# Kernel tuning notes

Hardware: AMD Instinct MI355X
Metric: run time of the kernel (lower is better)

## Reference

```python
import jax, jax.numpy as jnp
import numpy as np

EPS = 1e-12  # torch F.normalize eps
ALPHA = 100.0


def _l2norm(v, axis):
    n = jnp.sqrt(jnp.sum(v * v, axis=axis, keepdims=True))
    return v / jnp.maximum(n, EPS)


def setup_inputs() -> dict:
    key = jax.random.key(0)
    kx, kc = jax.random.split(key)
    B, D, H, W, K = 16, 512, 64, 64, 64
    x = jax.random.normal(kx, (B, D, H, W), dtype=jnp.float32)
    centroids = jax.random.uniform(kc, (K, D), dtype=jnp.float32)
    # NetVLAD._init_params: conv weight/bias derived from centroids at init
    conv_w = 2.0 * ALPHA * centroids                 # [K, D] (1x1 conv kernel)
    conv_b = -ALPHA * jnp.linalg.norm(centroids, axis=1)  # [K]
    return {"x": x, "centroids": centroids, "conv_w": conv_w, "conv_b": conv_b}


def reference(x, centroids, conv_w, conv_b):
    B, D = x.shape[:2]
    K = centroids.shape[0]
    # descriptor-wise L2 normalization over channel dim
    x = _l2norm(x, axis=1)
    xf = x.reshape(B, D, -1)                          # [B, D, N]
    # 1x1 conv == per-position matmul: [B, K, N]
    logits = jnp.einsum('kd,bdn->bkn', conv_w, xf) + conv_b[None, :, None]
    assign = jax.nn.softmax(logits, axis=1)           # soft assignment over K
    # vlad[b,k,d] = sum_n a[b,k,n]*(x[b,d,n] - c[k,d])
    #            = (a @ x^T) - a.sum(n) * c   (avoids B*K*D*N intermediate)
    agg = jnp.einsum('bkn,bdn->bkd', assign, xf)      # [B, K, D]
    mass = jnp.sum(assign, axis=-1)                   # [B, K]
    vlad = agg - mass[..., None] * centroids[None]    # [B, K, D]
    vlad = _l2norm(vlad, axis=2)                      # intra-normalization
    vlad = vlad.reshape(B, -1)                        # [B, K*D]
    return _l2norm(vlad, axis=1)
```

## Files before the change

kernel.cpp:

```cpp
#include <hip/hip_runtime.h>
#include <cstddef>

constexpr int Bn = 16, Dn = 512, Nn = 4096, Kn = 64;
constexpr int PN = 128;
constexpr int NP = Nn / PN;
constexpr int Dp = 520;
constexpr float FEPS = 1e-12f;

typedef __bf16 bf16x8 __attribute__((ext_vector_type(8)));
typedef float f32x4 __attribute__((ext_vector_type(4)));

__device__ __forceinline__ unsigned short bf_bits(__bf16 h) {
  union { __bf16 b; unsigned short u; } c;
  c.b = h;
  return c.u;
}

__global__ __launch_bounds__(256) void kW(const float* __restrict__ w,
                                          unsigned short* __restrict__ w_hi,
                                          unsigned short* __restrict__ w_lo) {
  const int idx = blockIdx.x * 256 + threadIdx.x;
  const float v = w[idx];
  const __bf16 h = (__bf16)v;
  const float r = v - (float)h;
  const __bf16 l = (__bf16)r;
  w_hi[idx] = bf_bits(h);
  w_lo[idx] = bf_bits(l);
}

__global__ __launch_bounds__(512, 4) void kF(const float* __restrict__ x,
                                             const unsigned short* __restrict__ w_hi,
                                             const unsigned short* __restrict__ w_lo,
                                             const float* __restrict__ conv_b,
                                             float* __restrict__ aggp,
                                             float* __restrict__ massp) {
  __shared__ float smem[2 * PN * 33];
  __shared__ float msum[8][64];
  const int tid = threadIdx.x;
  const int l = tid & 63;
  const int wv = tid >> 6;
  const int ll = l & 15;
  const int lg = l >> 4;
  const int b = blockIdx.x >> 5;
  const int p = blockIdx.x & 31;
  const int n0 = p << 7;
  const float* xb = x + (size_t)b * Dn * Nn + n0;

  f32x4 acc[4];
#pragma unroll
  for (int kt = 0; kt < 4; ++kt) acc[kt] = (f32x4){0.f, 0.f, 0.f, 0.f};
  float ss = 0.f;

  const int srow = tid >> 4;
  const int sc0 = (tid & 15) << 3;
  float4 pf0 = *(const float4*)(xb + (size_t)srow * Nn + sc0);
  float4 pf1 = *(const float4*)(xb + (size_t)srow * Nn + sc0 + 4);

  for (int dc = 0; dc < Dn; dc += 32) {
    float* xs = smem + ((dc >> 5) & 1) * (PN * 33);
    xs[(sc0 + 0) * 33 + srow] = pf0.x;
    xs[(sc0 + 1) * 33 + srow] = pf0.y;
    xs[(sc0 + 2) * 33 + srow] = pf0.z;
    xs[(sc0 + 3) * 33 + srow] = pf0.w;
    xs[(sc0 + 4) * 33 + srow] = pf1.x;
    xs[(sc0 + 5) * 33 + srow] = pf1.y;
    xs[(sc0 + 6) * 33 + srow] = pf1.z;
    xs[(sc0 + 7) * 33 + srow] = pf1.w;
    if (dc + 32 < Dn) {
      pf0 = *(const float4*)(xb + (size_t)(dc + 32 + srow) * Nn + sc0);
      pf1 = *(const float4*)(xb + (size_t)(dc + 32 + srow) * Nn + sc0 + 4);
    }
    __syncthreads();

    const int ncol = (wv << 4) + ll;
    const float* xcol = xs + ncol * 33 + lg * 8;
    float xv[8];
#pragma unroll
    for (int j = 0; j < 8; ++j) xv[j] = xcol[j];
    bf16x8 bh, bl;
#pragma unroll
    for (int j = 0; j < 8; ++j) {
      ss = fmaf(xv[j], xv[j], ss);
      const __bf16 h = (__bf16)xv[j];
      bh[j] = h;
      bl[j] = (__bf16)(xv[j] - (float)h);
    }
#pragma unroll
    for (int kt = 0; kt < 4; ++kt) {
      const size_t woff = (size_t)(kt * 16 + ll) * Dn + dc + lg * 8;
      bf16x8 ah = *(const bf16x8*)(w_hi + woff);
      bf16x8 al = *(const bf16x8*)(w_lo + woff);
      acc[kt] = __builtin_amdgcn_mfma_f32_16x16x32_bf16(ah, bh, acc[kt], 0, 0, 0);
      acc[kt] = __builtin_amdgcn_mfma_f32_16x16x32_bf16(ah, bl, acc[kt], 0, 0, 0);
      acc[kt] = __builtin_amdgcn_mfma_f32_16x16x32_bf16(al, bh, acc[kt], 0, 0, 0);
    }
  }

  ss += __shfl_xor(ss, 16);
  ss += __shfl_xor(ss, 32);
  const float iv = 1.f / fmaxf(sqrtf(ss), FEPS);
  float lgt[16];
#pragma unroll
  for (int kt = 0; kt < 4; ++kt)
#pragma unroll
    for (int r = 0; r < 4; ++r)
      lgt[kt * 4 + r] = fmaf(acc[kt][r], iv, conv_b[kt * 16 + lg * 4 + r]);
  float pmax = lgt[0];
#pragma unroll
  for (int i = 1; i < 16; ++i) pmax = fmaxf(pmax, lgt[i]);
  pmax = fmaxf(pmax, __shfl_xor(pmax, 16));
  pmax = fmaxf(pmax, __shfl_xor(pmax, 32));
  float ex[16];
  float psum = 0.f;
#pragma unroll
  for (int i = 0; i < 16; ++i) {
    ex[i] = expf(lgt[i] - pmax);
    psum += ex[i];
  }
  psum += __shfl_xor(psum, 16);
  psum += __shfl_xor(psum, 32);
  const float isum = 1.f / psum;

  __syncthreads();

  unsigned short* as_hi = (unsigned short*)smem;
  unsigned short* as_lo = as_hi + PN * Kn;
  const int ngb = (wv << 1) + (ll >> 3);
  const int jj = ll & 7;
#pragma unroll
  for (int i = 0; i < 16; ++i) {
    const int k = (i >> 2) * 16 + lg * 4 + (i & 3);
    const float a = ex[i] * isum;
    const float v = a * iv;
    const __bf16 h = (__bf16)v;
    as_hi[(ngb * 64 + k) * 8 + jj] = bf_bits(h);
    as_lo[(ngb * 64 + k) * 8 + jj] = bf_bits((__bf16)(v - (float)h));
    float m = a;
    m += __shfl_xor(m, 1);
    m += __shfl_xor(m, 2);
    m += __shfl_xor(m, 4);
    m += __shfl_xor(m, 8);
    if (ll == 0) msum[wv][k] = m;
  }
  __syncthreads();
  if (tid < 64) {
    float s = 0.f;
#pragma unroll
    for (int ww = 0; ww < 8; ++ww) s += msum[ww][tid];
    massp[((b << 5) + p) * Kn + tid] = s;
  }

  f32x4 acc2[4][4];
#pragma unroll
  for (int kt = 0; kt < 4; ++kt)
#pragma unroll
    for (int dt = 0; dt < 4; ++dt) acc2[kt][dt] = (f32x4){0.f, 0.f, 0.f, 0.f};

  const float* xq = x + (size_t)b * Dn * Nn +
                    (size_t)(wv * 64 + ll) * Nn + n0 + lg * 8;

#pragma unroll
  for (int nc = 0; nc < PN; nc += 32) {
    const int ng = (nc >> 3) + lg;
    bf16x8 af_h[4], af_l[4];
#pragma unroll
    for (int kt = 0; kt < 4; ++kt) {
      const int idx = (ng * 64 + kt * 16 + ll) * 8;
      af_h[kt] = *(const bf16x8*)(as_hi + idx);
      af_l[kt] = *(const bf16x8*)(as_lo + idx);
    }
    bf16x8 bx[4];
#pragma unroll
    for (int dt = 0; dt < 4; ++dt) {
      const float* xr = xq + (size_t)(dt * 16) * Nn + nc;
      float4 x0 = *(const float4*)(xr);
      float4 x1 = *(const float4*)(xr + 4);
      bx[dt][0] = (__bf16)x0.x; bx[dt][1] = (__bf16)x0.y;
      bx[dt][2] = (__bf16)x0.z; bx[dt][3] = (__bf16)x0.w;
      bx[dt][4] = (__bf16)x1.x; bx[dt][5] = (__bf16)x1.y;
      bx[dt][6] = (__bf16)x1.z; bx[dt][7] = (__bf16)x1.w;
    }
#pragma unroll
    for (int kt = 0; kt < 4; ++kt)
#pragma unroll
      for (int dt = 0; dt < 4; ++dt) {
        acc2[kt][dt] = __builtin_amdgcn_mfma_f32_16x16x32_bf16(
            af_h[kt], bx[dt], acc2[kt][dt], 0, 0, 0);
        acc2[kt][dt] = __builtin_amdgcn_mfma_f32_16x16x32_bf16(
            af_l[kt], bx[dt], acc2[kt][dt], 0, 0, 0);
      }
  }

  float* outb = aggp + (size_t)((b << 5) + p) * Kn * Dp;
#pragma unroll
  for (int kt = 0; kt < 4; ++kt)
#pragma unroll
    for (int dt = 0; dt < 4; ++dt) {
      const int krow = kt * 16 + (lg << 2);
      const int dcol = wv * 64 + dt * 16 + ll;
      float* op = outb + (size_t)krow * Dp + dcol;
#pragma unroll
      for (int r = 0; r < 4; ++r) op[(size_t)r * Dp] = acc2[kt][dt][r];
    }
}

__device__ __forceinline__ float blockReduceSum(float v, float* sb) {
#pragma unroll
  for (int off = 32; off > 0; off >>= 1) v += __shfl_down(v, off, 64);
  const int lane = threadIdx.x & 63, w = threadIdx.x >> 6;
  if (lane == 0) sb[w] = v;
  __syncthreads();
  if (threadIdx.x == 0) sb[4] = sb[0] + sb[1] + sb[2] + sb[3];
  __syncthreads();
  return sb[4];
}

__global__ __launch_bounds__(256) void kC1(const float* __restrict__ massp,
                                           const float* __restrict__ aggp,
                                           const float* __restrict__ centroids,
                                           float* __restrict__ out,
                                           float* __restrict__ rowsq) {
  __shared__ float sb[5];
  const int tid = threadIdx.x;
  const int b = blockIdx.x >> 6, k = blockIdx.x & 63;
  float s = 0.f;
  if (tid < 32) s = massp[((b << 5) + tid) * Kn + k];
  const float mass = blockReduceSum(s, sb);
  float v[2];
  float sq = 0.f;
#pragma unroll
  for (int u = 0; u < 2; ++u) {
    const int d = tid + (u << 8);
    float val = -mass * centroids[k * Dn + d];
#pragma unroll 8
    for (int pp = 0; pp < 32; ++pp)
      val += aggp[((size_t)((b << 5) + pp) * Kn + k) * Dp + d];
    v[u] = val;
    sq = fmaf(val, val, sq);
  }
  const float rsq = blockReduceSum(sq, sb);
  const float inv = 1.f / fmaxf(sqrtf(rsq), FEPS);
#pragma unroll
  for (int u = 0; u < 2; ++u)
    out[((size_t)b * Kn + k) * Dn + tid + (u << 8)] = v[u] * inv;
  if (tid == 0) rowsq[b * Kn + k] = rsq * inv * inv;
}

__global__ __launch_bounds__(256) void kC2(float* __restrict__ out,
                                           const float* __restrict__ rowsq) {
  __shared__ float sg;
  const int b = blockIdx.x, tid = threadIdx.x;
  float v = (tid < 64) ? rowsq[b * Kn + tid] : 0.f;
  if (tid < 64) {
#pragma unroll
    for (int off = 32; off > 0; off >>= 1) v += __shfl_down(v, off, 64);
  }
  if (tid == 0) sg = 1.f / fmaxf(sqrtf(v), FEPS);
  __syncthreads();
  const float inv = sg;
  float* ob = out + (size_t)b * (Kn * Dn);
  for (int t = tid; t < Kn * Dn; t += 256) ob[t] *= inv;
}

extern "C" void kernel_launch(void* const* d_in, const int* in_sizes, int n_in,
                              void* d_out, int out_size, void* d_ws,
                              size_t ws_size, hipStream_t stream) {
  const float* x = (const float*)d_in[0];
  const float* centroids = (const float*)d_in[1];
  const float* conv_w = (const float*)d_in[2];
  const float* conv_b = (const float*)d_in[3];
  float* out = (float*)d_out;
  float* ws = (float*)d_ws;
  float* aggp = ws;
  unsigned short* w_hi = (unsigned short*)(ws + 17039360);
  unsigned short* w_lo = (unsigned short*)(ws + 17055744);
  float* massp = ws + 17072128;
  float* rowsq = ws + 17104896;

  kW<<<128, 256, 0, stream>>>(conv_w, w_hi, w_lo);
  kF<<<512, 512, 0, stream>>>(x, w_hi, w_lo, conv_b, aggp, massp);
  kC1<<<1024, 256, 0, stream>>>(massp, aggp, centroids, out, rowsq);
  kC2<<<16, 256, 0, stream>>>(out, rowsq);
}
```

Baseline: 143.4 us.

## Stage 64-channel x tiles with two-deep register prefetch and fewer barriers

The x staging in the fused kernel now transposes 64 channels per step instead of 32, with two register prefetch sets that alternate between two shared buffers. This halves the number of barriers and gives each thread larger 16-float global loads. It also swaps __syncthreads for a raw lgkmcnt wait plus s_barrier. The costs are double the LDS footprint (about 67KB plus msum), which may cut occupancy under launch_bounds(512,4), and higher register pressure from 32 prefetch floats.

```diff
diff --git a/kernel.cpp b/kernel.cpp
--- a/kernel.cpp
+++ b/kernel.cpp
@@ -3,7 +3,6 @@
 
 constexpr int Bn = 16, Dn = 512, Nn = 4096, Kn = 64;
 constexpr int PN = 128;
-constexpr int NP = Nn / PN;
 constexpr int Dp = 520;
 constexpr float FEPS = 1e-12f;
 
@@ -34,7 +33,7 @@
                                              const float* __restrict__ conv_b,
                                              float* __restrict__ aggp,
                                              float* __restrict__ massp) {
-  __shared__ float smem[2 * PN * 33];
+  __shared__ float smem[2 * PN * 66];
   __shared__ float msum[8][64];
   const int tid = threadIdx.x;
   const int l = tid & 63;
@@ -51,50 +50,79 @@
   for (int kt = 0; kt < 4; ++kt) acc[kt] = (f32x4){0.f, 0.f, 0.f, 0.f};
   float ss = 0.f;
 
-  const int srow = tid >> 4;
-  const int sc0 = (tid & 15) << 3;
-  float4 pf0 = *(const float4*)(xb + (size_t)srow * Nn + sc0);
-  float4 pf1 = *(const float4*)(xb + (size_t)srow * Nn + sc0 + 4);
-
-  for (int dc = 0; dc < Dn; dc += 32) {
-    float* xs = smem + ((dc >> 5) & 1) * (PN * 33);
-    xs[(sc0 + 0) * 33 + srow] = pf0.x;
-    xs[(sc0 + 1) * 33 + srow] = pf0.y;
-    xs[(sc0 + 2) * 33 + srow] = pf0.z;
-    xs[(sc0 + 3) * 33 + srow] = pf0.w;
-    xs[(sc0 + 4) * 33 + srow] = pf1.x;
-    xs[(sc0 + 5) * 33 + srow] = pf1.y;
-    xs[(sc0 + 6) * 33 + srow] = pf1.z;
-    xs[(sc0 + 7) * 33 + srow] = pf1.w;
-    if (dc + 32 < Dn) {
-      pf0 = *(const float4*)(xb + (size_t)(dc + 32 + srow) * Nn + sc0);
-      pf1 = *(const float4*)(xb + (size_t)(dc + 32 + srow) * Nn + sc0 + 4);
-    }
-    __syncthreads();
-
-    const int ncol = (wv << 4) + ll;
-    const float* xcol = xs + ncol * 33 + lg * 8;
-    float xv[8];
-#pragma unroll
-    for (int j = 0; j < 8; ++j) xv[j] = xcol[j];
-    bf16x8 bh, bl;
-#pragma unroll
-    for (int j = 0; j < 8; ++j) {
-      ss = fmaf(xv[j], xv[j], ss);
-      const __bf16 h = (__bf16)xv[j];
-      bh[j] = h;
-      bl[j] = (__bf16)(xv[j] - (float)h);
-    }
-#pragma unroll
-    for (int kt = 0; kt < 4; ++kt) {
-      const size_t woff = (size_t)(kt * 16 + ll) * Dn + dc + lg * 8;
-      bf16x8 ah = *(const bf16x8*)(w_hi + woff);
-      bf16x8 al = *(const bf16x8*)(w_lo + woff);
-      acc[kt] = __builtin_amdgcn_mfma_f32_16x16x32_bf16(ah, bh, acc[kt], 0, 0, 0);
-      acc[kt] = __builtin_amdgcn_mfma_f32_16x16x32_bf16(ah, bl, acc[kt], 0, 0, 0);
-      acc[kt] = __builtin_amdgcn_mfma_f32_16x16x32_bf16(al, bh, acc[kt], 0, 0, 0);
-    }
-  }
+  const int srow = tid >> 3;
+  const int sc0 = (tid & 7) << 4;
+  const float* xsrc = xb + (size_t)srow * Nn + sc0;
+  const int ncol = (wv << 4) + ll;
+
+  float4 pfA[4], pfB[4];
+#pragma unroll
+  for (int q = 0; q < 4; ++q) pfA[q] = *(const float4*)(xsrc + 4 * q);
+#pragma unroll
+  for (int q = 0; q < 4; ++q)
+    pfB[q] = *(const float4*)(xsrc + (size_t)64 * Nn + 4 * q);
+
+#define KF_CONSUME(XS, DC)                                                    \
+  {                                                                           \
+    const float* xcol = (XS) + ncol * 66;                                     \
+    _Pragma("unroll") for (int s = 0; s < 2; ++s) {                           \
+      float xv[8];                                                            \
+      _Pragma("unroll") for (int j = 0; j < 8; ++j)                           \
+          xv[j] = xcol[s * 32 + lg * 8 + j];                                  \
+      bf16x8 bh, bl;                                                          \
+      _Pragma("unroll") for (int j = 0; j < 8; ++j) {                         \
+        ss = fmaf(xv[j], xv[j], ss);                                          \
+        const __bf16 h = (__bf16)xv[j];                                       \
+        bh[j] = h;                                                            \
+        bl[j] = (__bf16)(xv[j] - (float)h);                                   \
+      }                                                                       \
+      _Pragma("unroll") for (int kt = 0; kt < 4; ++kt) {                      \
+        const size_t woff = (size_t)(kt * 16 + ll) * Dn + (DC) + s * 32 + lg * 8; \
+        bf16x8 ah = *(const bf16x8*)(w_hi + woff);                            \
+        bf16x8 al = *(const bf16x8*)(w_lo + woff);                            \
+        acc[kt] = __builtin_amdgcn_mfma_f32_16x16x32_bf16(ah, bh, acc[kt], 0, 0, 0); \
+        acc[kt] = __builtin_amdgcn_mfma_f32_16x16x32_bf16(ah, bl, acc[kt], 0, 0, 0); \
+        acc[kt] = __builtin_amdgcn_mfma_f32_16x16x32_bf16(al, bh, acc[kt], 0, 0, 0); \
+      }                                                                       \
+    }                                                                         \
+  }
+
+#pragma unroll
+  for (int it = 0; it < 4; ++it) {
+    {
+      float* xs = smem;
+#pragma unroll
+      for (int q = 0; q < 4; ++q)
+#pragma unroll
+        for (int j = 0; j < 4; ++j)
+          xs[(sc0 + 4 * q + j) * 66 + srow] = ((const float*)&pfA[q])[j];
+      if (it < 3) {
+#pragma unroll
+        for (int q = 0; q < 4; ++q)
+          pfA[q] = *(const float4*)(xsrc + (size_t)(it * 128 + 128) * Nn + 4 * q);
+      }
+      asm volatile("s_waitcnt lgkmcnt(0)" ::: "memory");
+      __builtin_amdgcn_s_barrier();
+      KF_CONSUME(xs, it * 128);
+    }
+    {
+      float* xs = smem + PN * 66;
+#pragma unroll
+      for (int q = 0; q < 4; ++q)
+#pragma unroll
+        for (int j = 0; j < 4; ++j)
+          xs[(sc0 + 4 * q + j) * 66 + srow] = ((const float*)&pfB[q])[j];
+      if (it < 3) {
+#pragma unroll
+        for (int q = 0; q < 4; ++q)
+          pfB[q] = *(const float4*)(xsrc + (size_t)(it * 128 + 192) * Nn + 4 * q);
+      }
+      asm volatile("s_waitcnt lgkmcnt(0)" ::: "memory");
+      __builtin_amdgcn_s_barrier();
+      KF_CONSUME(xs, it * 128 + 64);
+    }
+  }
+#undef KF_CONSUME
 
   ss += __shfl_xor(ss, 16);
   ss += __shfl_xor(ss, 32);
```

Measured after the change: 150.1 us. 1.05x slower.

## Cache bf16 x tile in LDS, drop second x read, process two chunks per block

Applied to the files above, without the earlier changes.

The fused kernel now keeps a swizzled bf16 copy of the whole 512x128 x tile in LDS during the first pass. The aggregation GEMM reads x from LDS instead of reloading it from global memory. The low half of the assignment split is dropped, so the second GEMM uses single-bf16 assignments. Each block handles two N-chunks and accumulates them into one partial, which halves the partial aggregate buffer and the reduction work in kC1. The cost is a large LDS footprint (about 128KB), which lowers occupancy, plus a small loss of precision in the assignment weights.

```diff
diff --git a/kernel.cpp b/kernel.cpp
--- a/kernel.cpp
+++ b/kernel.cpp
@@ -3,7 +3,6 @@
 
 constexpr int Bn = 16, Dn = 512, Nn = 4096, Kn = 64;
 constexpr int PN = 128;
-constexpr int NP = Nn / PN;
 constexpr int Dp = 520;
 constexpr float FEPS = 1e-12f;
 
@@ -28,170 +27,164 @@
   w_lo[idx] = bf_bits(l);
 }
 
-__global__ __launch_bounds__(512, 4) void kF(const float* __restrict__ x,
+__global__ __launch_bounds__(512, 2) void kF(const float* __restrict__ x,
                                              const unsigned short* __restrict__ w_hi,
                                              const unsigned short* __restrict__ w_lo,
                                              const float* __restrict__ conv_b,
                                              float* __restrict__ aggp,
                                              float* __restrict__ massp) {
-  __shared__ float smem[2 * PN * 33];
+  __shared__ float xs[PN * 33];
+  __shared__ unsigned short xhi[Dn * PN];
   __shared__ float msum[8][64];
   const int tid = threadIdx.x;
   const int l = tid & 63;
   const int wv = tid >> 6;
   const int ll = l & 15;
   const int lg = l >> 4;
-  const int b = blockIdx.x >> 5;
-  const int p = blockIdx.x & 31;
-  const int n0 = p << 7;
-  const float* xb = x + (size_t)b * Dn * Nn + n0;
-
-  f32x4 acc[4];
-#pragma unroll
-  for (int kt = 0; kt < 4; ++kt) acc[kt] = (f32x4){0.f, 0.f, 0.f, 0.f};
-  float ss = 0.f;
-
+  const int b = blockIdx.x >> 4;
+  const int sp = blockIdx.x & 15;
   const int srow = tid >> 4;
   const int sc0 = (tid & 15) << 3;
-  float4 pf0 = *(const float4*)(xb + (size_t)srow * Nn + sc0);
-  float4 pf1 = *(const float4*)(xb + (size_t)srow * Nn + sc0 + 4);
-
-  for (int dc = 0; dc < Dn; dc += 32) {
-    float* xs = smem + ((dc >> 5) & 1) * (PN * 33);
-    xs[(sc0 + 0) * 33 + srow] = pf0.x;
-    xs[(sc0 + 1) * 33 + srow] = pf0.y;
-    xs[(sc0 + 2) * 33 + srow] = pf0.z;
-    xs[(sc0 + 3) * 33 + srow] = pf0.w;
-    xs[(sc0 + 4) * 33 + srow] = pf1.x;
-    xs[(sc0 + 5) * 33 + srow] = pf1.y;
-    xs[(sc0 + 6) * 33 + srow] = pf1.z;
-    xs[(sc0 + 7) * 33 + srow] = pf1.w;
-    if (dc + 32 < Dn) {
-      pf0 = *(const float4*)(xb + (size_t)(dc + 32 + srow) * Nn + sc0);
-      pf1 = *(const float4*)(xb + (size_t)(dc + 32 + srow) * Nn + sc0 + 4);
-    }
+  const int ncol = (wv << 4) + ll;
+
+  f32x4 acc2[4][4];
+#pragma unroll
+  for (int kt = 0; kt < 4; ++kt)
+#pragma unroll
+    for (int dt = 0; dt < 4; ++dt) acc2[kt][dt] = (f32x4){0.f, 0.f, 0.f, 0.f};
+
+  for (int rep = 0; rep < 2; ++rep) {
+    const int p = (sp << 1) + rep;
+    const int n0 = p << 7;
+    const float* xbp = x + (size_t)b * Dn * Nn + n0;
+
+    f32x4 acc[4];
+#pragma unroll
+    for (int kt = 0; kt < 4; ++kt) acc[kt] = (f32x4){0.f, 0.f, 0.f, 0.f};
+    float ss = 0.f;
+
+    float4 pf0 = *(const float4*)(xbp + (size_t)srow * Nn + sc0);
+    float4 pf1 = *(const float4*)(xbp + (size_t)srow * Nn + sc0 + 4);
+
+    for (int dc = 0; dc < Dn; dc += 32) {
+      const float pv[8] = {pf0.x, pf0.y, pf0.z, pf0.w, pf1.x, pf1.y, pf1.z, pf1.w};
+#pragma unroll
+      for (int j = 0; j < 8; ++j) xs[(sc0 + j) * 33 + srow] = pv[j];
+      {
+        unsigned short hb[8];
+#pragma unroll
+        for (int j = 0; j < 8; ++j) hb[j] = bf_bits((__bf16)pv[j]);
+        const unsigned byteoff =
+            (unsigned)(((dc + srow) * PN + sc0) * 2) ^ ((unsigned)(srow & 7) << 4);
+        uint4 hv;
+        hv.x = (unsigned)hb[0] | ((unsigned)hb[1] << 16);
+        hv.y = (unsigned)hb[2] | ((unsigned)hb[3] << 16);
+        hv.z = (unsigned)hb[4] | ((unsigned)hb[5] << 16);
+        hv.w = (unsigned)hb[6] | ((unsigned)hb[7] << 16);
+        *(uint4*)((char*)xhi + byteoff) = hv;
+      }
+      if (dc + 32 < Dn) {
+        pf0 = *(const float4*)(xbp + (size_t)(dc + 32 + srow) * Nn + sc0);
+        pf1 = *(const float4*)(xbp + (size_t)(dc + 32 + srow) * Nn + sc0 + 4);
+      }
+      asm volatile("s_waitcnt lgkmcnt(0)\ns_barrier" ::: "memory");
+
+      float xv[8];
+#pragma unroll
+      for (int j = 0; j < 8; ++j) xv[j] = xs[ncol * 33 + lg * 8 + j];
+      bf16x8 bh, bl;
+#pragma unroll
+      for (int j = 0; j < 8; ++j) {
+        ss = fmaf(xv[j], xv[j], ss);
+        const __bf16 h = (__bf16)xv[j];
+        bh[j] = h;
+        bl[j] = (__bf16)(xv[j] - (float)h);
+      }
+#pragma unroll
+      for (int kt = 0; kt < 4; ++kt) {
+        const size_t woff = (size_t)(kt * 16 + ll) * Dn + dc + lg * 8;
+        bf16x8 ah = *(const bf16x8*)(w_hi + woff);
+        bf16x8 al = *(const bf16x8*)(w_lo + woff);
+        acc[kt] = __builtin_amdgcn_mfma_f32_16x16x32_bf16(ah, bh, acc[kt], 0, 0, 0);
+        acc[kt] = __builtin_amdgcn_mfma_f32_16x16x32_bf16(ah, bl, acc[kt], 0, 0, 0);
+        acc[kt] = __builtin_amdgcn_mfma_f32_16x16x32_bf16(al, bh, acc[kt], 0, 0, 0);
+      }
+      asm volatile("s_waitcnt lgkmcnt(0)\ns_barrier" ::: "memory");
+    }
+
+    ss += __shfl_xor(ss, 16);
+    ss += __shfl_xor(ss, 32);
+    const float iv = 1.f / fmaxf(sqrtf(ss), FEPS);
+    float lgt[16];
+#pragma unroll
+    for (int kt = 0; kt < 4; ++kt)
+#pragma unroll
+      for (int r = 0; r < 4; ++r)
+        lgt[kt * 4 + r] = fmaf(acc[kt][r], iv, conv_b[kt * 16 + lg * 4 + r]);
+    float pmax = lgt[0];
+#pragma unroll
+    for (int i = 1; i < 16; ++i) pmax = fmaxf(pmax, lgt[i]);
+    pmax = fmaxf(pmax, __shfl_xor(pmax, 16));
+    pmax = fmaxf(pmax, __shfl_xor(pmax, 32));
+    float ex[16];
+    float psum = 0.f;
+#pragma unroll
+    for (int i = 0; i < 16; ++i) {
+      ex[i] = expf(lgt[i] - pmax);
+      psum += ex[i];
+    }
+    psum += __shfl_xor(psum, 16);
+    psum += __shfl_xor(psum, 32);
+    const float isum = 1.f / psum;
+
     __syncthreads();
 
-    const int ncol = (wv << 4) + ll;
-    const float* xcol = xs + ncol * 33 + lg * 8;
-    float xv[8];
-#pragma unroll
-    for (int j = 0; j < 8; ++j) xv[j] = xcol[j];
-    bf16x8 bh, bl;
-#pragma unroll
-    for (int j = 0; j < 8; ++j) {
-      ss = fmaf(xv[j], xv[j], ss);
-      const __bf16 h = (__bf16)xv[j];
-      bh[j] = h;
-      bl[j] = (__bf16)(xv[j] - (float)h);
-    }
-#pragma unroll
-    for (int kt = 0; kt < 4; ++kt) {
-      const size_t woff = (size_t)(kt * 16 + ll) * Dn + dc + lg * 8;
-      bf16x8 ah = *(const bf16x8*)(w_hi + woff);
-      bf16x8 al = *(const bf16x8*)(w_lo + woff);
-      acc[kt] = __builtin_amdgcn_mfma_f32_16x16x32_bf16(ah, bh, acc[kt], 0, 0, 0);
-      acc[kt] = __builtin_amdgcn_mfma_f32_16x16x32_bf16(ah, bl, acc[kt], 0, 0, 0);
-      acc[kt] = __builtin_amdgcn_mfma_f32_16x16x32_bf16(al, bh, acc[kt], 0, 0, 0);
-    }
+    unsigned short* as_hi = (unsigned short*)xs;
+    const int ngb = (wv << 1) + (ll >> 3);
+    const int jj = ll & 7;
+#pragma unroll
+    for (int i = 0; i < 16; ++i) {
+      const int k = (i >> 2) * 16 + lg * 4 + (i & 3);
+      const float a = ex[i] * isum;
+      as_hi[(ngb * 64 + k) * 8 + jj] = bf_bits((__bf16)(a * iv));
+      float m = a;
+      m += __shfl_xor(m, 1);
+      m += __shfl_xor(m, 2);
+      m += __shfl_xor(m, 4);
+      m += __shfl_xor(m, 8);
+      if (ll == 0) msum[wv][k] = m;
+    }
+    __syncthreads();
+    if (tid < 64) {
+      float s = 0.f;
+#pragma unroll
+      for (int ww = 0; ww < 8; ++ww) s += msum[ww][tid];
+      massp[((b << 5) + p) * Kn + tid] = s;
+    }
+
+#pragma unroll
+    for (int nc = 0; nc < PN; nc += 32) {
+      const int ng = (nc >> 3) + lg;
+      bf16x8 af[4];
+#pragma unroll
+      for (int kt = 0; kt < 4; ++kt)
+        af[kt] = *(const bf16x8*)(as_hi + (ng * 64 + kt * 16 + ll) * 8);
+#pragma unroll
+      for (int dt = 0; dt < 4; ++dt) {
+        const int d = wv * 64 + dt * 16 + ll;
+        const unsigned byteoff =
+            (unsigned)((d * PN + nc + lg * 8) * 2) ^ ((unsigned)(d & 7) << 4);
+        bf16x8 bx = *(const bf16x8*)((const char*)xhi + byteoff);
+#pragma unroll
+        for (int kt = 0; kt < 4; ++kt)
+          acc2[kt][dt] = __builtin_amdgcn_mfma_f32_16x16x32_bf16(
+              af[kt], bx, acc2[kt][dt], 0, 0, 0);
+      }
+    }
+    __syncthreads();
   }
 
-  ss += __shfl_xor(ss, 16);
-  ss += __shfl_xor(ss, 32);
-  const float iv = 1.f / fmaxf(sqrtf(ss), FEPS);
-  float lgt[16];
-#pragma unroll
-  for (int kt = 0; kt < 4; ++kt)
-#pragma unroll
-    for (int r = 0; r < 4; ++r)
-      lgt[kt * 4 + r] = fmaf(acc[kt][r], iv, conv_b[kt * 16 + lg * 4 + r]);
-  float pmax = lgt[0];
-#pragma unroll
-  for (int i = 1; i < 16; ++i) pmax = fmaxf(pmax, lgt[i]);
-  pmax = fmaxf(pmax, __shfl_xor(pmax, 16));
-  pmax = fmaxf(pmax, __shfl_xor(pmax, 32));
-  float ex[16];
-  float psum = 0.f;
-#pragma unroll
-  for (int i = 0; i < 16; ++i) {
-    ex[i] = expf(lgt[i] - pmax);
-    psum += ex[i];
-  }
-  psum += __shfl_xor(psum, 16);
-  psum += __shfl_xor(psum, 32);
-  const float isum = 1.f / psum;
-
-  __syncthreads();
-
-  unsigned short* as_hi = (unsigned short*)smem;
-  unsigned short* as_lo = as_hi + PN * Kn;
-  const int ngb = (wv << 1) + (ll >> 3);
-  const int jj = ll & 7;
-#pragma unroll
-  for (int i = 0; i < 16; ++i) {
-    const int k = (i >> 2) * 16 + lg * 4 + (i & 3);
-    const float a = ex[i] * isum;
-    const float v = a * iv;
-    const __bf16 h = (__bf16)v;
-    as_hi[(ngb * 64 + k) * 8 + jj] = bf_bits(h);
-    as_lo[(ngb * 64 + k) * 8 + jj] = bf_bits((__bf16)(v - (float)h));
-    float m = a;
-    m += __shfl_xor(m, 1);
-    m += __shfl_xor(m, 2);
-    m += __shfl_xor(m, 4);
-    m += __shfl_xor(m, 8);
-    if (ll == 0) msum[wv][k] = m;
-  }
-  __syncthreads();
-  if (tid < 64) {
-    float s = 0.f;
-#pragma unroll
-    for (int ww = 0; ww < 8; ++ww) s += msum[ww][tid];
-    massp[((b << 5) + p) * Kn + tid] = s;
-  }
-
-  f32x4 acc2[4][4];
-#pragma unroll
-  for (int kt = 0; kt < 4; ++kt)
-#pragma unroll
-    for (int dt = 0; dt < 4; ++dt) acc2[kt][dt] = (f32x4){0.f, 0.f, 0.f, 0.f};
-
-  const float* xq = x + (size_t)b * Dn * Nn +
-                    (size_t)(wv * 64 + ll) * Nn + n0 + lg * 8;
-
-#pragma unroll
-  for (int nc = 0; nc < PN; nc += 32) {
-    const int ng = (nc >> 3) + lg;
-    bf16x8 af_h[4], af_l[4];
-#pragma unroll
-    for (int kt = 0; kt < 4; ++kt) {
-      const int idx = (ng * 64 + kt * 16 + ll) * 8;
-      af_h[kt] = *(const bf16x8*)(as_hi + idx);
-      af_l[kt] = *(const bf16x8*)(as_lo + idx);
-    }
-    bf16x8 bx[4];
-#pragma unroll
-    for (int dt = 0; dt < 4; ++dt) {
-      const float* xr = xq + (size_t)(dt * 16) * Nn + nc;
-      float4 x0 = *(const float4*)(xr);
-      float4 x1 = *(const float4*)(xr + 4);
-      bx[dt][0] = (__bf16)x0.x; bx[dt][1] = (__bf16)x0.y;
-      bx[dt][2] = (__bf16)x0.z; bx[dt][3] = (__bf16)x0.w;
-      bx[dt][4] = (__bf16)x1.x; bx[dt][5] = (__bf16)x1.y;
-      bx[dt][6] = (__bf16)x1.z; bx[dt][7] = (__bf16)x1.w;
-    }
-#pragma unroll
-    for (int kt = 0; kt < 4; ++kt)
-#pragma unroll
-      for (int dt = 0; dt < 4; ++dt) {
-        acc2[kt][dt] = __builtin_amdgcn_mfma_f32_16x16x32_bf16(
-            af_h[kt], bx[dt], acc2[kt][dt], 0, 0, 0);
-        acc2[kt][dt] = __builtin_amdgcn_mfma_f32_16x16x32_bf16(
-            af_l[kt], bx[dt], acc2[kt][dt], 0, 0, 0);
-      }
-  }
-
-  float* outb = aggp + (size_t)((b << 5) + p) * Kn * Dp;
+  float* outb = aggp + (size_t)((b << 4) + sp) * Kn * Dp;
 #pragma unroll
   for (int kt = 0; kt < 4; ++kt)
 #pragma unroll
@@ -232,9 +225,9 @@
   for (int u = 0; u < 2; ++u) {
     const int d = tid + (u << 8);
     float val = -mass * centroids[k * Dn + d];
-#pragma unroll 8
-    for (int pp = 0; pp < 32; ++pp)
-      val += aggp[((size_t)((b << 5) + pp) * Kn + k) * Dp + d];
+#pragma unroll
+    for (int pp = 0; pp < 16; ++pp)
+      val += aggp[((size_t)((b << 4) + pp) * Kn + k) * Dp + d];
     v[u] = val;
     sq = fmaf(val, val, sq);
   }
@@ -272,13 +265,13 @@
   float* out = (float*)d_out;
   float* ws = (float*)d_ws;
   float* aggp = ws;
-  unsigned short* w_hi = (unsigned short*)(ws + 17039360);
-  unsigned short* w_lo = (unsigned short*)(ws + 17055744);
-  float* massp = ws + 17072128;
-  float* rowsq = ws + 17104896;
+  unsigned short* w_hi = (unsigned short*)(ws + 8519680);
+  unsigned short* w_lo = (unsigned short*)(ws + 8536064);
+  float* massp = ws + 8552448;
+  float* rowsq = ws + 8585216;
 
   kW<<<128, 256, 0, stream>>>(conv_w, w_hi, w_lo);
-  kF<<<512, 512, 0, stream>>>(x, w_hi, w_lo, conv_b, aggp, massp);
+  kF<<<256, 512, 0, stream>>>(x, w_hi, w_lo, conv_b, aggp, massp);
   kC1<<<1024, 256, 0, stream>>>(massp, aggp, centroids, out, rowsq);
   kC2<<<16, 256, 0, stream>>>(out, rowsq);
 }
```

After: 123.2 us. 1.16x faster.

## Use per-wave private transpose tiles and drop low-bf16 split in aggregation GEMM

Applied to the files above, without the earlier changes.

Each wave now loads and transposes only its own 16 columns of x into a private double-buffered LDS tile, which removes the block-wide __syncthreads in the first GEMM loop and the prefetch registers. The assignment matrix for the second GEMM is stored only as a single bf16 term, halving its MFMAs and LDS traffic. Dropping the low part reduces accuracy of the aggregation. Global loads are no longer prefetched one iteration ahead, so latency hiding relies on occupancy and unrolling.

```diff
diff --git a/kernel.cpp b/kernel.cpp
--- a/kernel.cpp
+++ b/kernel.cpp
@@ -3,7 +3,6 @@
 
 constexpr int Bn = 16, Dn = 512, Nn = 4096, Kn = 64;
 constexpr int PN = 128;
-constexpr int NP = Nn / PN;
 constexpr int Dp = 520;
 constexpr float FEPS = 1e-12f;
 
@@ -34,7 +33,8 @@
                                              const float* __restrict__ conv_b,
                                              float* __restrict__ aggp,
                                              float* __restrict__ massp) {
-  __shared__ float smem[2 * PN * 33];
+  __shared__ float tiles[8 * 2 * 528];
+  __shared__ unsigned short as_hi[PN * Kn];
   __shared__ float msum[8][64];
   const int tid = threadIdx.x;
   const int l = tid & 63;
@@ -44,39 +44,34 @@
   const int b = blockIdx.x >> 5;
   const int p = blockIdx.x & 31;
   const int n0 = p << 7;
-  const float* xb = x + (size_t)b * Dn * Nn + n0;
+  const int lrow = l >> 1;
+  const int lcol = (l & 1) << 3;
+  const float* xw = x + (size_t)b * Dn * Nn + n0 + (wv << 4) + lcol;
+  float* const tbase = tiles + wv * (2 * 528);
 
   f32x4 acc[4];
 #pragma unroll
   for (int kt = 0; kt < 4; ++kt) acc[kt] = (f32x4){0.f, 0.f, 0.f, 0.f};
   float ss = 0.f;
 
-  const int srow = tid >> 4;
-  const int sc0 = (tid & 15) << 3;
-  float4 pf0 = *(const float4*)(xb + (size_t)srow * Nn + sc0);
-  float4 pf1 = *(const float4*)(xb + (size_t)srow * Nn + sc0 + 4);
-
-  for (int dc = 0; dc < Dn; dc += 32) {
-    float* xs = smem + ((dc >> 5) & 1) * (PN * 33);
-    xs[(sc0 + 0) * 33 + srow] = pf0.x;
-    xs[(sc0 + 1) * 33 + srow] = pf0.y;
-    xs[(sc0 + 2) * 33 + srow] = pf0.z;
-    xs[(sc0 + 3) * 33 + srow] = pf0.w;
-    xs[(sc0 + 4) * 33 + srow] = pf1.x;
-    xs[(sc0 + 5) * 33 + srow] = pf1.y;
-    xs[(sc0 + 6) * 33 + srow] = pf1.z;
-    xs[(sc0 + 7) * 33 + srow] = pf1.w;
-    if (dc + 32 < Dn) {
-      pf0 = *(const float4*)(xb + (size_t)(dc + 32 + srow) * Nn + sc0);
-      pf1 = *(const float4*)(xb + (size_t)(dc + 32 + srow) * Nn + sc0 + 4);
-    }
-    __syncthreads();
-
-    const int ncol = (wv << 4) + ll;
-    const float* xcol = xs + ncol * 33 + lg * 8;
+#pragma unroll 2
+  for (int it = 0; it < 16; ++it) {
+    const int dc = it << 5;
+    float* tw = tbase + (it & 1) * 528;
+    const float* src = xw + (size_t)(dc + lrow) * Nn;
+    float4 a0 = *(const float4*)(src);
+    float4 a1 = *(const float4*)(src + 4);
+    tw[(lcol + 0) * 33 + lrow] = a0.x;
+    tw[(lcol + 1) * 33 + lrow] = a0.y;
+    tw[(lcol + 2) * 33 + lrow] = a0.z;
+    tw[(lcol + 3) * 33 + lrow] = a0.w;
+    tw[(lcol + 4) * 33 + lrow] = a1.x;
+    tw[(lcol + 5) * 33 + lrow] = a1.y;
+    tw[(lcol + 6) * 33 + lrow] = a1.z;
+    tw[(lcol + 7) * 33 + lrow] = a1.w;
     float xv[8];
 #pragma unroll
-    for (int j = 0; j < 8; ++j) xv[j] = xcol[j];
+    for (int j = 0; j < 8; ++j) xv[j] = tw[ll * 33 + lg * 8 + j];
     bf16x8 bh, bl;
 #pragma unroll
     for (int j = 0; j < 8; ++j) {
@@ -121,20 +116,13 @@
   psum += __shfl_xor(psum, 32);
   const float isum = 1.f / psum;
 
-  __syncthreads();
-
-  unsigned short* as_hi = (unsigned short*)smem;
-  unsigned short* as_lo = as_hi + PN * Kn;
   const int ngb = (wv << 1) + (ll >> 3);
   const int jj = ll & 7;
 #pragma unroll
   for (int i = 0; i < 16; ++i) {
     const int k = (i >> 2) * 16 + lg * 4 + (i & 3);
     const float a = ex[i] * isum;
-    const float v = a * iv;
-    const __bf16 h = (__bf16)v;
-    as_hi[(ngb * 64 + k) * 8 + jj] = bf_bits(h);
-    as_lo[(ngb * 64 + k) * 8 + jj] = bf_bits((__bf16)(v - (float)h));
+    as_hi[(ngb * 64 + k) * 8 + jj] = bf_bits((__bf16)(a * iv));
     float m = a;
     m += __shfl_xor(m, 1);
     m += __shfl_xor(m, 2);
@@ -162,13 +150,10 @@
 #pragma unroll
   for (int nc = 0; nc < PN; nc += 32) {
     const int ng = (nc >> 3) + lg;
-    bf16x8 af_h[4], af_l[4];
-#pragma unroll
-    for (int kt = 0; kt < 4; ++kt) {
-      const int idx = (ng * 64 + kt * 16 + ll) * 8;
-      af_h[kt] = *(const bf16x8*)(as_hi + idx);
-      af_l[kt] = *(const bf16x8*)(as_lo + idx);
-    }
+    bf16x8 af[4];
+#pragma unroll
+    for (int kt = 0; kt < 4; ++kt)
+      af[kt] = *(const bf16x8*)(as_hi + (ng * 64 + kt * 16 + ll) * 8);
     bf16x8 bx[4];
 #pragma unroll
     for (int dt = 0; dt < 4; ++dt) {
@@ -183,12 +168,9 @@
 #pragma unroll
     for (int kt = 0; kt < 4; ++kt)
 #pragma unroll
-      for (int dt = 0; dt < 4; ++dt) {
+      for (int dt = 0; dt < 4; ++dt)
         acc2[kt][dt] = __builtin_amdgcn_mfma_f32_16x16x32_bf16(
-            af_h[kt], bx[dt], acc2[kt][dt], 0, 0, 0);
-        acc2[kt][dt] = __builtin_amdgcn_mfma_f32_16x16x32_bf16(
-            af_l[kt], bx[dt], acc2[kt][dt], 0, 0, 0);
-      }
+            af[kt], bx[dt], acc2[kt][dt], 0, 0, 0);
   }
 
   float* outb = aggp + (size_t)((b << 5) + p) * Kn * Dp;
```

Measured after the change: 140.0 us. -2.3%, faster.
